# Optimization experiments

Measured on AMD Instinct MI355X. Metric: run time of the kernel, lower is better.

The kernel has to match this reference:

```python
import jax, jax.numpy as jnp
import numpy as np

TEMPERATURE = 1.0
STRIDE = 1
PADDING = 2
RF = 5  # receptive_field_size
TREE_DEPTH = 3

# Each of the 16 binary difflogic ops op_g(a,b) is multilinear:
# op_g = c0 + c1*a + c2*b + c3*a*b. Rows ordered per the standard difflogic table:
# 0:0, 1:a&b, 2:a&~b, 3:a, 4:~a&b, 5:b, 6:xor, 7:or, 8:nor, 9:xnor,
# 10:~b, 11:a|~b, 12:~a, 13:~a|b, 14:nand, 15:1
_C = jnp.asarray(np.array([
    [0, 0, 0, 0],
    [0, 0, 0, 1],
    [0, 1, 0, -1],
    [0, 1, 0, 0],
    [0, 0, 1, -1],
    [0, 0, 1, 0],
    [0, 1, 1, -2],
    [0, 1, 1, -1],
    [1, -1, -1, 1],
    [1, -1, -1, 2],
    [1, 0, -1, 0],
    [1, 0, -1, 1],
    [1, -1, 0, 0],
    [1, -1, 0, 1],
    [1, 0, 0, -1],
    [1, 0, 0, 0]], dtype=np.float32))


def _gate(a, b, logits):
    """Soft LUT gate. a,b: (B,K,N,P); logits: (N,K,16) -> (B,K,N,P)."""
    w = jax.nn.softmax(logits / TEMPERATURE, axis=-1)          # (N,K,16)
    coef = jnp.einsum('nkg,gc->knc', w, _C)                    # (K,N,4)
    c = coef[None, :, :, None, :]                              # (1,K,N,1,4)
    return c[..., 0] + c[..., 1] * a + c[..., 2] * b + c[..., 3] * (a * b)


def setup_inputs() -> dict:
    key = jax.random.key(0)
    ks = jax.random.split(key, 8)
    B, Cin, H, W = 16, 32, 64, 64
    K, N = 64, 2 ** TREE_DEPTH  # num_kernels, leaf gates per tree
    x = jax.random.uniform(ks[0], (B, Cin, H, W), dtype=jnp.float32)
    idx_h = jax.random.randint(ks[1], (2, K, N), 0, RF, dtype=jnp.int32)
    idx_w = jax.random.randint(ks[2], (2, K, N), 0, RF, dtype=jnp.int32)
    idx_c = jax.random.randint(ks[3], (2, K, N), 0, Cin, dtype=jnp.int32)
    w0 = jax.random.normal(ks[4], (8, K, 16), dtype=jnp.float32)
    w1 = jax.random.normal(ks[5], (4, K, 16), dtype=jnp.float32)
    w2 = jax.random.normal(ks[6], (2, K, 16), dtype=jnp.float32)
    w3 = jax.random.normal(ks[7], (1, K, 16), dtype=jnp.float32)
    return {"x": x, "idx_h": idx_h, "idx_w": idx_w, "idx_c": idx_c,
            "w0": w0, "w1": w1, "w2": w2, "w3": w3}


def reference(x, idx_h, idx_w, idx_c, w0, w1, w2, w3):
    B, Cin, H, W = x.shape
    xp = jnp.pad(x, ((0, 0), (0, 0), (PADDING, PADDING), (PADDING, PADDING)))
    out_h = (H + 2 * PADDING - RF) // STRIDE + 1
    out_w = (W + 2 * PADDING - RF) // STRIDE + 1
    # Absolute gather coords per (rank-slot, kernel, leaf-gate, out_y, out_x)
    abs_h = idx_h[..., None, None] + (jnp.arange(out_h) * STRIDE)[:, None]   # (2,K,N,oh,1)
    abs_w = idx_w[..., None, None] + (jnp.arange(out_w) * STRIDE)[None, :]   # (2,K,N,1,ow)
    cc = idx_c[..., None, None]                                              # (2,K,N,1,1)
    g = xp[:, cc, abs_h, abs_w]                                # (B,2,K,N,oh,ow)
    K, N = g.shape[2], g.shape[3]
    g = g.reshape(B, 2, K, N, out_h * out_w)                   # (B,2,K,N,P)
    cur = _gate(g[:, 0], g[:, 1], w0)                          # (B,K,8,P) leaf level
    for wl in (w1, w2, w3):                                    # reduce tree: 8->4->2->1
        cur = _gate(cur[:, :, 0::2, :], cur[:, :, 1::2, :], wl)
    return cur.reshape(B, K, out_h, out_w)
```

## Files before the change

### kernel.cpp

```cpp
#include <hip/hip_runtime.h>
#include <hip/hip_bf16.h>

#define CIN 32
#define HW 64
#define KK 64
#define NLEAF 8
#define PADDING 2
#define TH 4
#define TCW 16
#define WR 8
#define WC 20
#define WPOS (CIN * WR * WC)

typedef float f32x2 __attribute__((ext_vector_type(2)));

__device__ __constant__ float d_C[16][4] = {
    {0, 0, 0, 0},  {0, 0, 0, 1},  {0, 1, 0, -1}, {0, 1, 0, 0},
    {0, 0, 1, -1}, {0, 0, 1, 0},  {0, 1, 1, -2}, {0, 1, 1, -1},
    {1, -1, -1, 1},{1, -1, -1, 2},{1, 0, -1, 0}, {1, 0, -1, 1},
    {1, -1, 0, 0}, {1, -1, 0, 1}, {1, 0, 0, -1}, {1, 0, 0, 0}
};

__global__ __launch_bounds__(256) void prep_kernel(
    const int* __restrict__ idx_h, const int* __restrict__ idx_w, const int* __restrict__ idx_c,
    const float* __restrict__ w0, const float* __restrict__ w1,
    const float* __restrict__ w2, const float* __restrict__ w3,
    float* __restrict__ coefA, int* __restrict__ loffA)
{
    if (blockIdx.x == 4) {
        int k = threadIdx.x;
        if (k < KK) {
            #pragma unroll
            for (int n = 0; n < 16; ++n) {
                int s = n >> 3, leaf = n & 7;
                int o = s * (KK * NLEAF) + k * NLEAF + leaf;
                loffA[k * 16 + n] = (idx_c[o] * (WR * WC) + idx_h[o] * WC + idx_w[o]) * 8;
            }
        }
        return;
    }
    int t = blockIdx.x * blockDim.x + threadIdx.x;
    if (t >= KK * 15) return;
    int k = t / 15, node = t % 15;
    const float* wp; int n;
    if (node < 8)       { wp = w0; n = node; }
    else if (node < 12) { wp = w1; n = node - 8; }
    else if (node < 14) { wp = w2; n = node - 12; }
    else                { wp = w3; n = 0; }
    const float* l = wp + (n * KK + k) * 16;
    float m = l[0];
    #pragma unroll
    for (int g = 1; g < 16; ++g) m = fmaxf(m, l[g]);
    float p[16], s = 0.f;
    #pragma unroll
    for (int g = 0; g < 16; ++g) { p[g] = expf(l[g] - m); s += p[g]; }
    float inv = 1.f / s;
    float c0 = 0, c1 = 0, c2 = 0, c3 = 0;
    #pragma unroll
    for (int g = 0; g < 16; ++g) {
        float w = p[g] * inv;
        c0 = fmaf(w, d_C[g][0], c0);
        c1 = fmaf(w, d_C[g][1], c1);
        c2 = fmaf(w, d_C[g][2], c2);
        c3 = fmaf(w, d_C[g][3], c3);
    }
    float* o = coefA + (k * 60 + node * 4);
    o[0] = c0; o[1] = c1; o[2] = c2; o[3] = c3;
}

__device__ __forceinline__ f32x2 bc(float s) { return (f32x2){s, s}; }
__device__ __forceinline__ f32x2 gate2(const float* c, f32x2 a, f32x2 b) {
    return __builtin_elementwise_fma(b,
               __builtin_elementwise_fma(a, bc(c[3]), bc(c[2])),
               __builtin_elementwise_fma(a, bc(c[1]), bc(c[0])));
}

__global__ __launch_bounds__(512) void logic_conv_kernel(
    const float* __restrict__ x, const int* __restrict__ loffA,
    const float* __restrict__ coefA, float* __restrict__ out)
{
    __shared__ f32x2 xt[WPOS];

    int tid = threadIdx.x;
    int bp  = blockIdx.x & 7;
    int t   = blockIdx.x >> 3;
    int r0  = (t >> 2) * TH;
    int c0  = (t & 3) * TCW;

    const float* xb0 = x + (size_t)(2 * bp) * (CIN * HW * HW);
    const float* xb1 = xb0 + (CIN * HW * HW);

    #pragma unroll
    for (int i = 0; i < 10; ++i) {
        int e  = tid + i * 512;
        int c  = e / (WR * WC);
        int r  = e - c * (WR * WC);
        int rr = r / WC;
        int cc = r - rr * WC;
        int ih = r0 + rr - PADDING, iw = c0 + cc - PADDING;
        f32x2 v = {0.f, 0.f};
        if ((unsigned)ih < HW && (unsigned)iw < HW) {
            int go = (c * HW + ih) * HW + iw;
            v.x = xb0[go];
            v.y = xb1[go];
        }
        xt[e] = v;
    }
    __syncthreads();

    int lane = tid & 63, wave = tid >> 6;
    int tr = lane >> 4, tc = lane & 15;
    int pxb   = (tr * WC + tc) * 8;
    int pxout = (r0 + tr) * HW + (c0 + tc);
    float* outB0 = out + ((size_t)(2 * bp) << 18);
    float* outB1 = outB0 + (1 << 18);
    const char* xtb = (const char*)xt;

    int k0 = __builtin_amdgcn_readfirstlane(wave << 3);

    #pragma unroll 2
    for (int i = 0; i < 8; ++i) {
        int k = k0 + i;
        const int*   L = loffA + (k << 4);
        const float* C = coefA + k * 60;

        f32x2 g[16];
        #pragma unroll
        for (int n = 0; n < 16; ++n)
            g[n] = *(const f32x2*)(xtb + (L[n] + pxb));

        f32x2 v[8];
        #pragma unroll
        for (int n = 0; n < 8; ++n)
            v[n] = gate2(C + 4 * n, g[n], g[8 + n]);
        f32x2 u[4];
        #pragma unroll
        for (int n = 0; n < 4; ++n)
            u[n] = gate2(C + 32 + 4 * n, v[2 * n], v[2 * n + 1]);
        f32x2 t0 = gate2(C + 48, u[0], u[1]);
        f32x2 t1 = gate2(C + 52, u[2], u[3]);
        f32x2 r  = gate2(C + 56, t0, t1);

        int ko = (k << 12) + pxout;
        __builtin_nontemporal_store(r.x, &outB0[ko]);
        __builtin_nontemporal_store(r.y, &outB1[ko]);
    }
}

extern "C" void kernel_launch(void* const* d_in, const int* in_sizes, int n_in,
                              void* d_out, int out_size, void* d_ws, size_t ws_size,
                              hipStream_t stream) {
    const float* x     = (const float*)d_in[0];
    const int*   idx_h = (const int*)d_in[1];
    const int*   idx_w = (const int*)d_in[2];
    const int*   idx_c = (const int*)d_in[3];
    const float* w0    = (const float*)d_in[4];
    const float* w1    = (const float*)d_in[5];
    const float* w2    = (const float*)d_in[6];
    const float* w3    = (const float*)d_in[7];
    float* out   = (float*)d_out;

    float* coefA = (float*)d_ws;
    int*   loffA = (int*)((char*)d_ws + 16384);

    hipLaunchKernelGGL(prep_kernel, dim3(5), dim3(256), 0, stream,
                       idx_h, idx_w, idx_c, w0, w1, w2, w3, coefA, loffA);
    hipLaunchKernelGGL(logic_conv_kernel, dim3(512), dim3(512), 0, stream,
                       x, loffA, coefA, out);
}
```

Baseline: 21.38 us.

## Use taller spatial tiles and split kernels across blocks for more parallelism

New measurement: 25.03 us. 17.1% more time.

```diff
diff --git a/kernel.cpp b/kernel.cpp
--- a/kernel.cpp
+++ b/kernel.cpp
@@ -6,9 +6,9 @@
 #define KK 64
 #define NLEAF 8
 #define PADDING 2
-#define TH 4
-#define TCW 16
-#define WR 8
+#define TR 8
+#define TC 16
+#define WR 12
 #define WC 20
 #define WPOS (CIN * WR * WC)
 
@@ -34,7 +34,7 @@
             for (int n = 0; n < 16; ++n) {
                 int s = n >> 3, leaf = n & 7;
                 int o = s * (KK * NLEAF) + k * NLEAF + leaf;
-                loffA[k * 16 + n] = (idx_c[o] * (WR * WC) + idx_h[o] * WC + idx_w[o]) * 8;
+                loffA[k * 16 + n] = idx_c[o] * (WR * WC) + idx_h[o] * WC + idx_w[o];
             }
         }
         return;
@@ -75,7 +75,7 @@
                __builtin_elementwise_fma(a, bc(c[1]), bc(c[0])));
 }
 
-__global__ __launch_bounds__(512) void logic_conv_kernel(
+__global__ __launch_bounds__(512, 4) void logic_conv_kernel(
     const float* __restrict__ x, const int* __restrict__ loffA,
     const float* __restrict__ coefA, float* __restrict__ out)
 {
@@ -83,15 +83,17 @@
 
     int tid = threadIdx.x;
     int bp  = blockIdx.x & 7;
-    int t   = blockIdx.x >> 3;
-    int r0  = (t >> 2) * TH;
-    int c0  = (t & 3) * TCW;
+    int rem = blockIdx.x >> 3;
+    int t   = rem & 31;
+    int kg  = rem >> 5;
+    int r0  = (t >> 2) * TR;
+    int c0  = (t & 3) * TC;
 
     const float* xb0 = x + (size_t)(2 * bp) * (CIN * HW * HW);
     const float* xb1 = xb0 + (CIN * HW * HW);
 
     #pragma unroll
-    for (int i = 0; i < 10; ++i) {
+    for (int i = 0; i < 15; ++i) {
         int e  = tid + i * 512;
         int c  = e / (WR * WC);
         int r  = e - c * (WR * WC);
@@ -110,40 +112,42 @@
 
     int lane = tid & 63, wave = tid >> 6;
     int tr = lane >> 4, tc = lane & 15;
-    int pxb   = (tr * WC + tc) * 8;
+    int pxe   = tr * WC + tc;
     int pxout = (r0 + tr) * HW + (c0 + tc);
     float* outB0 = out + ((size_t)(2 * bp) << 18);
     float* outB1 = outB0 + (1 << 18);
-    const char* xtb = (const char*)xt;
 
-    int k0 = __builtin_amdgcn_readfirstlane(wave << 3);
+    int kbase = __builtin_amdgcn_readfirstlane(kg * 16 + wave * 2);
 
-    #pragma unroll 2
-    for (int i = 0; i < 8; ++i) {
-        int k = k0 + i;
+    #pragma unroll
+    for (int p = 0; p < 2; ++p) {
+        int k = kbase + p;
         const int*   L = loffA + (k << 4);
         const float* C = coefA + k * 60;
 
-        f32x2 g[16];
         #pragma unroll
-        for (int n = 0; n < 16; ++n)
-            g[n] = *(const f32x2*)(xtb + (L[n] + pxb));
+        for (int it = 0; it < 2; ++it) {
+            f32x2 g[16];
+            #pragma unroll
+            for (int n = 0; n < 16; ++n)
+                g[n] = xt[L[n] + pxe + it * (4 * WC)];
 
-        f32x2 v[8];
-        #pragma unroll
-        for (int n = 0; n < 8; ++n)
-            v[n] = gate2(C + 4 * n, g[n], g[8 + n]);
-        f32x2 u[4];
-        #pragma unroll
-        for (int n = 0; n < 4; ++n)
-            u[n] = gate2(C + 32 + 4 * n, v[2 * n], v[2 * n + 1]);
-        f32x2 t0 = gate2(C + 48, u[0], u[1]);
-        f32x2 t1 = gate2(C + 52, u[2], u[3]);
-        f32x2 r  = gate2(C + 56, t0, t1);
+            f32x2 v[8];
+            #pragma unroll
+            for (int n = 0; n < 8; ++n)
+                v[n] = gate2(C + 4 * n, g[n], g[8 + n]);
+            f32x2 u[4];
+            #pragma unroll
+            for (int n = 0; n < 4; ++n)
+                u[n] = gate2(C + 32 + 4 * n, v[2 * n], v[2 * n + 1]);
+            f32x2 t0 = gate2(C + 48, u[0], u[1]);
+            f32x2 t1 = gate2(C + 52, u[2], u[3]);
+            f32x2 r  = gate2(C + 56, t0, t1);
 
-        int ko = (k << 12) + pxout;
-        __builtin_nontemporal_store(r.x, &outB0[ko]);
-        __builtin_nontemporal_store(r.y, &outB1[ko]);
+            int ko = (k << 12) + pxout + it * (4 * HW);
+            __builtin_nontemporal_store(r.x, &outB0[ko]);
+            __builtin_nontemporal_store(r.y, &outB1[ko]);
+        }
     }
 }
 
@@ -165,6 +169,6 @@
 
     hipLaunchKernelGGL(prep_kernel, dim3(5), dim3(256), 0, stream,
                        idx_h, idx_w, idx_c, w0, w1, w2, w3, coefA, loffA);
-    hipLaunchKernelGGL(logic_conv_kernel, dim3(512), dim3(512), 0, stream,
+    hipLaunchKernelGGL(logic_conv_kernel, dim3(1024), dim3(512), 0, stream,
                        x, loffA, coefA, out);
 }
```

## Retile to square 8x8 pixel tiles and split kernels across two blocks

Applied to the files above, without the earlier changes.

Result: slower. 25.40 us (+18.8%).

```diff
diff --git a/kernel.cpp b/kernel.cpp
--- a/kernel.cpp
+++ b/kernel.cpp
@@ -6,11 +6,9 @@
 #define KK 64
 #define NLEAF 8
 #define PADDING 2
-#define TH 4
-#define TCW 16
-#define WR 8
-#define WC 20
-#define WPOS (CIN * WR * WC)
+#define TT 8
+#define WS 12
+#define WPOS (CIN * WS * WS)
 
 typedef float f32x2 __attribute__((ext_vector_type(2)));
 
@@ -27,45 +25,45 @@
     const float* __restrict__ w2, const float* __restrict__ w3,
     float* __restrict__ coefA, int* __restrict__ loffA)
 {
-    if (blockIdx.x == 4) {
-        int k = threadIdx.x;
-        if (k < KK) {
-            #pragma unroll
-            for (int n = 0; n < 16; ++n) {
-                int s = n >> 3, leaf = n & 7;
-                int o = s * (KK * NLEAF) + k * NLEAF + leaf;
-                loffA[k * 16 + n] = (idx_c[o] * (WR * WC) + idx_h[o] * WC + idx_w[o]) * 8;
-            }
+    int tid = blockIdx.x * 256 + threadIdx.x;
+
+    {
+        int k = tid >> 4, j = tid & 15;
+        int s = j & 1, leaf = j >> 1;
+        int o = s * (KK * NLEAF) + k * NLEAF + leaf;
+        loffA[tid] = idx_c[o] * (WS * WS) + idx_h[o] * WS + idx_w[o];
+    }
+
+    if (tid < KK * 15) {
+        int k = tid / 15, node = tid % 15;
+        const float* wp; int n;
+        if (node < 8)       { wp = w0; n = node; }
+        else if (node < 12) { wp = w1; n = node - 8; }
+        else if (node < 14) { wp = w2; n = node - 12; }
+        else                { wp = w3; n = 0; }
+        const float4* lp = (const float4*)(wp + (size_t)(n * KK + k) * 16);
+        float4 L0 = lp[0], L1 = lp[1], L2 = lp[2], L3 = lp[3];
+        float l[16] = {L0.x, L0.y, L0.z, L0.w, L1.x, L1.y, L1.z, L1.w,
+                       L2.x, L2.y, L2.z, L2.w, L3.x, L3.y, L3.z, L3.w};
+        float m = l[0];
+        #pragma unroll
+        for (int g = 1; g < 16; ++g) m = fmaxf(m, l[g]);
+        float p[16], s = 0.f;
+        #pragma unroll
+        for (int g = 0; g < 16; ++g) { p[g] = __expf(l[g] - m); s += p[g]; }
+        float inv = 1.f / s;
+        float c0 = 0, c1 = 0, c2 = 0, c3 = 0;
+        #pragma unroll
+        for (int g = 0; g < 16; ++g) {
+            float w = p[g] * inv;
+            c0 = fmaf(w, d_C[g][0], c0);
+            c1 = fmaf(w, d_C[g][1], c1);
+            c2 = fmaf(w, d_C[g][2], c2);
+            c3 = fmaf(w, d_C[g][3], c3);
         }
-        return;
+        float* o = coefA + (k * 60 + node * 4);
+        o[0] = c0; o[1] = c1; o[2] = c2; o[3] = c3;
     }
-    int t = blockIdx.x * blockDim.x + threadIdx.x;
-    if (t >= KK * 15) return;
-    int k = t / 15, node = t % 15;
-    const float* wp; int n;
-    if (node < 8)       { wp = w0; n = node; }
-    else if (node < 12) { wp = w1; n = node - 8; }
-    else if (node < 14) { wp = w2; n = node - 12; }
-    else                { wp = w3; n = 0; }
-    const float* l = wp + (n * KK + k) * 16;
-    float m = l[0];
-    #pragma unroll
-    for (int g = 1; g < 16; ++g) m = fmaxf(m, l[g]);
-    float p[16], s = 0.f;
-    #pragma unroll
-    for (int g = 0; g < 16; ++g) { p[g] = expf(l[g] - m); s += p[g]; }
-    float inv = 1.f / s;
-    float c0 = 0, c1 = 0, c2 = 0, c3 = 0;
-    #pragma unroll
-    for (int g = 0; g < 16; ++g) {
-        float w = p[g] * inv;
-        c0 = fmaf(w, d_C[g][0], c0);
-        c1 = fmaf(w, d_C[g][1], c1);
-        c2 = fmaf(w, d_C[g][2], c2);
-        c3 = fmaf(w, d_C[g][3], c3);
-    }
-    float* o = coefA + (k * 60 + node * 4);
-    o[0] = c0; o[1] = c1; o[2] = c2; o[3] = c3;
 }
 
 __device__ __forceinline__ f32x2 bc(float s) { return (f32x2){s, s}; }
@@ -75,7 +73,7 @@
                __builtin_elementwise_fma(a, bc(c[1]), bc(c[0])));
 }
 
-__global__ __launch_bounds__(512) void logic_conv_kernel(
+__global__ __launch_bounds__(512, 8) void logic_conv_kernel(
     const float* __restrict__ x, const int* __restrict__ loffA,
     const float* __restrict__ coefA, float* __restrict__ out)
 {
@@ -83,20 +81,22 @@
 
     int tid = threadIdx.x;
     int bp  = blockIdx.x & 7;
-    int t   = blockIdx.x >> 3;
-    int r0  = (t >> 2) * TH;
-    int c0  = (t & 3) * TCW;
+    int rem = blockIdx.x >> 3;
+    int t   = rem & 63;
+    int kh  = rem >> 6;
+    int r0  = (t >> 3) * TT;
+    int c0  = (t & 7) * TT;
 
     const float* xb0 = x + (size_t)(2 * bp) * (CIN * HW * HW);
     const float* xb1 = xb0 + (CIN * HW * HW);
 
     #pragma unroll
-    for (int i = 0; i < 10; ++i) {
+    for (int i = 0; i < 9; ++i) {
         int e  = tid + i * 512;
-        int c  = e / (WR * WC);
-        int r  = e - c * (WR * WC);
-        int rr = r / WC;
-        int cc = r - rr * WC;
+        int c  = e / (WS * WS);
+        int r  = e - c * (WS * WS);
+        int rr = r / WS;
+        int cc = r - rr * WS;
         int ih = r0 + rr - PADDING, iw = c0 + cc - PADDING;
         f32x2 v = {0.f, 0.f};
         if ((unsigned)ih < HW && (unsigned)iw < HW) {
@@ -109,30 +109,27 @@
     __syncthreads();
 
     int lane = tid & 63, wave = tid >> 6;
-    int tr = lane >> 4, tc = lane & 15;
-    int pxb   = (tr * WC + tc) * 8;
+    int tr = lane >> 3, tc = lane & 7;
+    int pxe   = tr * WS + tc;
     int pxout = (r0 + tr) * HW + (c0 + tc);
     float* outB0 = out + ((size_t)(2 * bp) << 18);
     float* outB1 = outB0 + (1 << 18);
-    const char* xtb = (const char*)xt;
 
-    int k0 = __builtin_amdgcn_readfirstlane(wave << 3);
+    int kbase = __builtin_amdgcn_readfirstlane(kh * 32 + wave * 4);
 
     #pragma unroll 2
-    for (int i = 0; i < 8; ++i) {
-        int k = k0 + i;
+    for (int i = 0; i < 4; ++i) {
+        int k = kbase + i;
         const int*   L = loffA + (k << 4);
         const float* C = coefA + k * 60;
 
-        f32x2 g[16];
-        #pragma unroll
-        for (int n = 0; n < 16; ++n)
-            g[n] = *(const f32x2*)(xtb + (L[n] + pxb));
-
         f32x2 v[8];
         #pragma unroll
-        for (int n = 0; n < 8; ++n)
-            v[n] = gate2(C + 4 * n, g[n], g[8 + n]);
+        for (int n = 0; n < 8; ++n) {
+            f32x2 ga = xt[L[2 * n]     + pxe];
+            f32x2 gb = xt[L[2 * n + 1] + pxe];
+            v[n] = gate2(C + 4 * n, ga, gb);
+        }
         f32x2 u[4];
         #pragma unroll
         for (int n = 0; n < 4; ++n)
@@ -163,8 +160,8 @@
     float* coefA = (float*)d_ws;
     int*   loffA = (int*)((char*)d_ws + 16384);
 
-    hipLaunchKernelGGL(prep_kernel, dim3(5), dim3(256), 0, stream,
+    hipLaunchKernelGGL(prep_kernel, dim3(4), dim3(256), 0, stream,
                        idx_h, idx_w, idx_c, w0, w1, w2, w3, coefA, loffA);
-    hipLaunchKernelGGL(logic_conv_kernel, dim3(512), dim3(512), 0, stream,
+    hipLaunchKernelGGL(logic_conv_kernel, dim3(1024), dim3(512), 0, stream,
                        x, loffA, coefA, out);
 }
```
